# Performance work log

Hardware: AMD Instinct MI355X
Metric: run time of the kernel (lower is better)

## Reference

```python
import jax, jax.numpy as jnp
import numpy as np

N_NODES = 100000


def setup_inputs() -> dict:
    key = jax.random.key(0)
    k1, k2, k3 = jax.random.split(key, 3)
    x = jax.random.normal(k1, (N_NODES, 128), dtype=jnp.float32)
    edge_index = jax.random.randint(k2, (2, 1600000), 0, N_NODES, dtype=jnp.int32)
    # GCNConv linear weight: [out_features, in_features], bias: [out_features]
    W = jax.random.normal(k3, (128, 128), dtype=jnp.float32) * (1.0 / np.sqrt(128.0))
    b = jnp.zeros((128,), dtype=jnp.float32)
    return {"x": x, "edge_index": edge_index, "W": W, "b": b}


def reference(x, edge_index, W, b):
    n = x.shape[0]
    # --- add self loops (PyG GCNConv default) ---
    loop = jnp.arange(n, dtype=edge_index.dtype)
    row = jnp.concatenate([edge_index[0], loop])  # source nodes
    col = jnp.concatenate([edge_index[1], loop])  # target nodes
    # --- symmetric degree normalization D^{-1/2} A_hat D^{-1/2} ---
    ones = jnp.ones(row.shape[0], dtype=x.dtype)
    deg = jax.ops.segment_sum(ones, col, num_segments=n)
    deg_inv_sqrt = jnp.where(deg > 0, jax.lax.rsqrt(deg), 0.0)
    norm = deg_inv_sqrt[row] * deg_inv_sqrt[col]  # [E + N]
    # --- linear transform then gather-normalize-scatter aggregation ---
    xw = x @ W.T  # [N, out]
    msgs = xw[row] * norm[:, None]  # [E + N, out]
    out = jax.ops.segment_sum(msgs, col, num_segments=n)  # [N, out]
    return out + b
```

## Files before the change

### kernel.cpp

```cpp
#include <hip/hip_runtime.h>

#define NF 128
#define WLD2 136

#define BSHIFT 7
#define BNODES (1 << BSHIFT)
#define NBUCK 782
#define BCAP 2560
#define CHUNK 4096

typedef __attribute__((ext_vector_type(8))) short bf16x8;
typedef __attribute__((ext_vector_type(4))) float f32x4;

__device__ inline short f2bf_rne(float f) {
    unsigned u = __float_as_uint(f);
    u += 0x7FFFu + ((u >> 16) & 1u);
    return (short)(u >> 16);
}
__device__ inline float bf_lo(unsigned u) { return __uint_as_float(u << 16); }
__device__ inline float bf_hi(unsigned u) { return __uint_as_float(u & 0xFFFF0000u); }

__global__ void binit_kernel(int* __restrict__ bcursor) {
    int i = blockIdx.x * blockDim.x + threadIdx.x;
    if (i < NBUCK) bcursor[i] = i * BCAP;
}

__global__ __launch_bounds__(256) void bucketize_kernel(const int* __restrict__ row,
                                                        const int* __restrict__ col,
                                                        int* __restrict__ bcursor,
                                                        int* __restrict__ bpacked, int E) {
    __shared__ int2 pe[CHUNK];
    __shared__ int hist[NBUCK];
    __shared__ int base[NBUCK];
    const int t = threadIdx.x;
    const int e0 = blockIdx.x * CHUNK;
    const int cnt = min(CHUNK, E - e0);
    for (int i = t; i < NBUCK; i += 256) hist[i] = 0;
    __syncthreads();
    for (int i = t; i < cnt; i += 256) {
        int c = col[e0 + i];
        int r = row[e0 + i];
        pe[i] = make_int2(c, r);
        atomicAdd(&hist[c >> BSHIFT], 1);
    }
    __syncthreads();
    for (int i = t; i < NBUCK; i += 256) {
        int h = hist[i];
        base[i] = h ? atomicAdd(&bcursor[i], h) : 0;
        hist[i] = 0;
    }
    __syncthreads();
    for (int i = t; i < cnt; i += 256) {
        int2 p = pe[i];
        int bk = p.x >> BSHIFT;
        int pos = base[bk] + atomicAdd(&hist[bk], 1);
        bpacked[pos] = (p.y << BSHIFT) | (p.x & (BNODES - 1));
    }
}

__device__ inline int block_exclusive_scan_256(int val) {
    __shared__ int wsum[4];
    int lane = threadIdx.x & 63, wave = threadIdx.x >> 6;
    int x = val;
#pragma unroll
    for (int off = 1; off < 64; off <<= 1) {
        int y = __shfl_up(x, off, 64);
        if (lane >= off) x += y;
    }
    if (lane == 63) wsum[wave] = x;
    __syncthreads();
    if (threadIdx.x == 0) {
        int acc = 0;
        for (int w = 0; w < 4; ++w) { int t = wsum[w]; wsum[w] = acc; acc += t; }
    }
    __syncthreads();
    return x - val + wsum[wave];
}

__global__ __launch_bounds__(256) void bucket_build_kernel(const int* __restrict__ bpacked,
                                                           const int* __restrict__ bcursor,
                                                           int* __restrict__ cnt,
                                                           float* __restrict__ dis,
                                                           int* __restrict__ offs,
                                                           int* __restrict__ ed, int N) {
    __shared__ int pe[BCAP];
    __shared__ int h[BNODES];
    __shared__ int edl[BCAP];
    const int b = blockIdx.x;
    const int node0 = b << BSHIFT;
    const int nn = min(BNODES, N - node0);
    const int start = b * BCAP;
    const int ecnt = bcursor[b] - start;
    for (int i = threadIdx.x; i < nn; i += 256) h[i] = 0;
    __syncthreads();
    for (int i = threadIdx.x; i < ecnt; i += 256) {
        int p = bpacked[start + i];
        pe[i] = p;
        atomicAdd(&h[p & (BNODES - 1)], 1);
    }
    __syncthreads();
    const int t = threadIdx.x;
    int v0 = (2 * t < nn) ? h[2 * t] : 0;
    int v1 = (2 * t + 1 < nn) ? h[2 * t + 1] : 0;
    int exc = block_exclusive_scan_256(v0 + v1);
    if (2 * t < nn) {
        offs[node0 + 2 * t] = start + exc;
        cnt[node0 + 2 * t] = v0;
        dis[node0 + 2 * t] = rsqrtf((float)v0 + 1.0f);
        h[2 * t] = exc;
    }
    if (2 * t + 1 < nn) {
        offs[node0 + 2 * t + 1] = start + exc + v0;
        cnt[node0 + 2 * t + 1] = v1;
        dis[node0 + 2 * t + 1] = rsqrtf((float)v1 + 1.0f);
        h[2 * t + 1] = exc + v0;
    }
    __syncthreads();
    for (int i = threadIdx.x; i < ecnt; i += 256) {
        int p = pe[i];
        int pos = atomicAdd(&h[p & (BNODES - 1)], 1);
        edl[pos] = p >> BSHIFT;
    }
    __syncthreads();
    for (int i = threadIdx.x; i < ecnt; i += 256) ed[start + i] = edl[i];
}

__global__ __launch_bounds__(256) void gemm_xws_kernel(const float* __restrict__ x,
                                                       const float* __restrict__ W,
                                                       const float* __restrict__ dis,
                                                       unsigned short* __restrict__ xws,
                                                       int n) {
    __shared__ short Wl[NF * WLD2];

    for (int idx = threadIdx.x; idx < NF * 32; idx += 256) {
        int o = idx >> 5;
        int kq = (idx & 31) << 2;
        float4 v = *(const float4*)(W + o * NF + kq);
        short* d = &Wl[o * WLD2 + kq];
        d[0] = f2bf_rne(v.x); d[1] = f2bf_rne(v.y);
        d[2] = f2bf_rne(v.z); d[3] = f2bf_rne(v.w);
    }
    __syncthreads();

    const int lane = threadIdx.x & 63;
    const int wave = threadIdx.x >> 6;
    const int mbase = wave * 32;
    const int l15 = lane & 15;
    const int quad = lane >> 4;
    const int tile = blockIdx.x * 128;

    f32x4 acc[2][8];
#pragma unroll
    for (int mb = 0; mb < 2; ++mb)
#pragma unroll
        for (int nb = 0; nb < 8; ++nb) acc[mb][nb] = (f32x4)0.0f;

#pragma unroll
    for (int kc = 0; kc < 4; ++kc) {
        const int kof = kc * 32 + quad * 8;
        bf16x8 Bf[8];
#pragma unroll
        for (int nb = 0; nb < 8; ++nb) {
            int o = nb * 16 + l15;
            Bf[nb] = *(const bf16x8*)(&Wl[o * WLD2 + kof]);
        }
#pragma unroll
        for (int mb = 0; mb < 2; ++mb) {
            int r = tile + mbase + mb * 16 + l15;
            if (r >= n) r = n - 1;
            const float4* ap = (const float4*)(x + (size_t)r * NF + kof);
            float4 a0 = ap[0], a1 = ap[1];
            bf16x8 Af;
            Af[0] = f2bf_rne(a0.x); Af[1] = f2bf_rne(a0.y);
            Af[2] = f2bf_rne(a0.z); Af[3] = f2bf_rne(a0.w);
            Af[4] = f2bf_rne(a1.x); Af[5] = f2bf_rne(a1.y);
            Af[6] = f2bf_rne(a1.z); Af[7] = f2bf_rne(a1.w);
#pragma unroll
            for (int nb = 0; nb < 8; ++nb)
                acc[mb][nb] = __builtin_amdgcn_mfma_f32_16x16x32_bf16(Af, Bf[nb], acc[mb][nb], 0, 0, 0);
        }
    }

#pragma unroll
    for (int mb = 0; mb < 2; ++mb) {
        int rbase = tile + mbase + mb * 16 + quad * 4;
#pragma unroll
        for (int reg = 0; reg < 4; ++reg) {
            int r = rbase + reg;
            if (r < n) {
                float dsc = dis[r];
#pragma unroll
                for (int nb = 0; nb < 8; ++nb) {
                    int c = nb * 16 + l15;
                    xws[(size_t)r * NF + c] = (unsigned short)f2bf_rne(acc[mb][nb][reg] * dsc);
                }
            }
        }
    }
}

__global__ __launch_bounds__(256) void gather_kernel(const int* __restrict__ ed,
                                                     const int* __restrict__ offs,
                                                     const int* __restrict__ cnt,
                                                     const float* __restrict__ dis,
                                                     const unsigned short* __restrict__ xws,
                                                     const float* __restrict__ b,
                                                     float* __restrict__ out,
                                                     int nbase, int nend) {
    int node = nbase + (int)((blockIdx.x * blockDim.x + threadIdx.x) >> 6);
    const int lane = threadIdx.x & 63;
    if (node >= nend) return;
    node = __builtin_amdgcn_readfirstlane(node);
    const int lsub = lane & 31;
    const bool lo = lane < 32;
    const float dc = dis[node];
    const int start = offs[node];
    const int end = start + cnt[node];

    float ax = 0.f, ay = 0.f, az = 0.f, aw = 0.f;
    {
        uint2 u = *(const uint2*)(xws + (size_t)node * NF + lsub * 4);
        if (lo) { ax = bf_lo(u.x); ay = bf_hi(u.x); az = bf_lo(u.y); aw = bf_hi(u.y); }
    }
    int i = start;
    for (; i + 16 <= end; i += 16) {
        int r0 = ed[i], r1 = ed[i + 1], r2 = ed[i + 2], r3 = ed[i + 3];
        int r4 = ed[i + 4], r5 = ed[i + 5], r6 = ed[i + 6], r7 = ed[i + 7];
        int r8 = ed[i + 8], r9 = ed[i + 9], ra = ed[i + 10], rb = ed[i + 11];
        int rc = ed[i + 12], rd = ed[i + 13], re = ed[i + 14], rf = ed[i + 15];
        int sa = lo ? r0 : r1, sb = lo ? r2 : r3, sc = lo ? r4 : r5, sd = lo ? r6 : r7;
        int se = lo ? r8 : r9, sf = lo ? ra : rb, sg = lo ? rc : rd, sh = lo ? re : rf;
        uint2 ua = *(const uint2*)(xws + (size_t)sa * NF + lsub * 4);
        uint2 ub = *(const uint2*)(xws + (size_t)sb * NF + lsub * 4);
        uint2 uc = *(const uint2*)(xws + (size_t)sc * NF + lsub * 4);
        uint2 ud = *(const uint2*)(xws + (size_t)sd * NF + lsub * 4);
        uint2 ue = *(const uint2*)(xws + (size_t)se * NF + lsub * 4);
        uint2 uf = *(const uint2*)(xws + (size_t)sf * NF + lsub * 4);
        uint2 ug = *(const uint2*)(xws + (size_t)sg * NF + lsub * 4);
        uint2 uh = *(const uint2*)(xws + (size_t)sh * NF + lsub * 4);
        ax += bf_lo(ua.x) + bf_lo(ub.x) + bf_lo(uc.x) + bf_lo(ud.x);
        ay += bf_hi(ua.x) + bf_hi(ub.x) + bf_hi(uc.x) + bf_hi(ud.x);
        az += bf_lo(ua.y) + bf_lo(ub.y) + bf_lo(uc.y) + bf_lo(ud.y);
        aw += bf_hi(ua.y) + bf_hi(ub.y) + bf_hi(uc.y) + bf_hi(ud.y);
        ax += bf_lo(ue.x) + bf_lo(uf.x) + bf_lo(ug.x) + bf_lo(uh.x);
        ay += bf_hi(ue.x) + bf_hi(uf.x) + bf_hi(ug.x) + bf_hi(uh.x);
        az += bf_lo(ue.y) + bf_lo(uf.y) + bf_lo(ug.y) + bf_lo(uh.y);
        aw += bf_hi(ue.y) + bf_hi(uf.y) + bf_hi(ug.y) + bf_hi(uh.y);
    }
    for (; i < end; i += 8) {
        int i1 = min(i + 1, end - 1), i2 = min(i + 2, end - 1), i3 = min(i + 3, end - 1);
        int i4 = min(i + 4, end - 1), i5 = min(i + 5, end - 1), i6 = min(i + 6, end - 1),
            i7 = min(i + 7, end - 1);
        int r0 = ed[i], r1 = ed[i1], r2 = ed[i2], r3 = ed[i3];
        int r4 = ed[i4], r5 = ed[i5], r6 = ed[i6], r7 = ed[i7];
        int sa = lo ? r0 : r1, sb = lo ? r2 : r3, sc = lo ? r4 : r5, sd = lo ? r6 : r7;
        uint2 ua = *(const uint2*)(xws + (size_t)sa * NF + lsub * 4);
        uint2 ub = *(const uint2*)(xws + (size_t)sb * NF + lsub * 4);
        uint2 uc = *(const uint2*)(xws + (size_t)sc * NF + lsub * 4);
        uint2 ud = *(const uint2*)(xws + (size_t)sd * NF + lsub * 4);
        const int my0 = lo ? 0 : 1;
        if (i + my0 < end)     { ax += bf_lo(ua.x); ay += bf_hi(ua.x); az += bf_lo(ua.y); aw += bf_hi(ua.y); }
        if (i + 2 + my0 < end) { ax += bf_lo(ub.x); ay += bf_hi(ub.x); az += bf_lo(ub.y); aw += bf_hi(ub.y); }
        if (i + 4 + my0 < end) { ax += bf_lo(uc.x); ay += bf_hi(uc.x); az += bf_lo(uc.y); aw += bf_hi(uc.y); }
        if (i + 6 + my0 < end) { ax += bf_lo(ud.x); ay += bf_hi(ud.x); az += bf_lo(ud.y); aw += bf_hi(ud.y); }
    }
    ax += __shfl_xor(ax, 32, 64);
    ay += __shfl_xor(ay, 32, 64);
    az += __shfl_xor(az, 32, 64);
    aw += __shfl_xor(aw, 32, 64);
    if (lo) {
        float4 bb = ((const float4*)b)[lsub];
        float4 o;
        o.x = fmaf(ax, dc, bb.x);
        o.y = fmaf(ay, dc, bb.y);
        o.z = fmaf(az, dc, bb.z);
        o.w = fmaf(aw, dc, bb.w);
        ((float4*)(out + (size_t)node * NF))[lsub] = o;
    }
}

extern "C" void kernel_launch(void* const* d_in, const int* in_sizes, int n_in,
                              void* d_out, int out_size, void* d_ws, size_t ws_size,
                              hipStream_t stream) {
    const float* x = (const float*)d_in[0];
    const int* ei = (const int*)d_in[1];
    const float* W = (const float*)d_in[2];
    const float* b = (const float*)d_in[3];
    float* out = (float*)d_out;

    const int N = in_sizes[0] / NF;
    const int E = in_sizes[1] / 2;
    const int* row = ei;
    const int* col = ei + E;

    char* ws = (char*)d_ws;
    unsigned short* xws = (unsigned short*)ws;
    ws += (size_t)N * NF * sizeof(unsigned short);
    int* cnt = (int*)ws; ws += (size_t)N * sizeof(int);
    float* dis = (float*)ws; ws += (size_t)N * sizeof(float);
    int* offs = (int*)ws; ws += (size_t)N * sizeof(int);
    int* bpacked = (int*)ws; ws += (size_t)NBUCK * BCAP * sizeof(int);
    int* bcursor = (int*)ws; ws += 1024 * sizeof(int);
    int* ed = (int*)ws;

    const int CB = (E + CHUNK - 1) / CHUNK;

    binit_kernel<<<(NBUCK + 255) / 256, 256, 0, stream>>>(bcursor);
    bucketize_kernel<<<CB, 256, 0, stream>>>(row, col, bcursor, bpacked, E);

    bucket_build_kernel<<<NBUCK, 256, 0, stream>>>(bpacked, bcursor, cnt, dis, offs, ed, N);

    gemm_xws_kernel<<<(N + 127) / 128, 256, 0, stream>>>(x, W, dis, xws, N);

    {
        int half = (N / 2 + 3) & ~3;
        int blocks1 = (half + 3) / 4;
        int blocks2 = (N - half + 3) / 4;
        gather_kernel<<<blocks1, 256, 0, stream>>>(ed, offs, cnt, dis, xws, b, out, 0, half);
        gather_kernel<<<blocks2, 256, 0, stream>>>(ed, offs, cnt, dis, xws, b, out, half, N);
    }
}
```

Before: 220.0 us.

## Pre-swizzle bf16 weights once and shrink GEMM tiles to 64 rows

A prep kernel, folded into the bucket cursor init, converts W to bf16 once in MFMA fragment order. Each GEMM block then copies that swizzled layout into LDS with a plain vector copy, instead of converting fp32 W per block with padded strides. Each block now handles 64 rows with one 16-row MFMA tile per wave, and all x loads are issued up front. This is meant to cut per-block W conversion cost and register pressure and to improve occupancy and latency hiding. The cost is twice as many blocks, each reloading the 32KB W tile.

```diff
diff --git a/kernel.cpp b/kernel.cpp
--- a/kernel.cpp
+++ b/kernel.cpp
@@ -1,7 +1,6 @@
 #include <hip/hip_runtime.h>
 
 #define NF 128
-#define WLD2 136
 
 #define BSHIFT 7
 #define BNODES (1 << BSHIFT)
@@ -20,9 +19,25 @@
 __device__ inline float bf_lo(unsigned u) { return __uint_as_float(u << 16); }
 __device__ inline float bf_hi(unsigned u) { return __uint_as_float(u & 0xFFFF0000u); }
 
-__global__ void binit_kernel(int* __restrict__ bcursor) {
-    int i = blockIdx.x * blockDim.x + threadIdx.x;
-    if (i < NBUCK) bcursor[i] = i * BCAP;
+__global__ __launch_bounds__(256) void prep_kernel(const float* __restrict__ W,
+                                                   unsigned short* __restrict__ wswz,
+                                                   int* __restrict__ bcursor) {
+    int t = blockIdx.x * 256 + threadIdx.x;
+    if (t < NBUCK) bcursor[t] = t * BCAP;
+    if (t < 2048) {
+        int lane = t & 63, frag = t >> 6;
+        int nb = frag & 7, kc = frag >> 3;
+        int o = nb * 16 + (lane & 15);
+        int k0 = kc * 32 + (lane >> 4) * 8;
+        const float4* ap = (const float4*)(W + o * NF + k0);
+        float4 a0 = ap[0], a1 = ap[1];
+        bf16x8 v;
+        v[0] = f2bf_rne(a0.x); v[1] = f2bf_rne(a0.y);
+        v[2] = f2bf_rne(a0.z); v[3] = f2bf_rne(a0.w);
+        v[4] = f2bf_rne(a1.x); v[5] = f2bf_rne(a1.y);
+        v[6] = f2bf_rne(a1.z); v[7] = f2bf_rne(a1.w);
+        *(bf16x8*)(wswz + (size_t)t * 8) = v;
+    }
 }
 
 __global__ __launch_bounds__(256) void bucketize_kernel(const int* __restrict__ row,
@@ -126,75 +141,60 @@
 }
 
 __global__ __launch_bounds__(256) void gemm_xws_kernel(const float* __restrict__ x,
-                                                       const float* __restrict__ W,
+                                                       const unsigned short* __restrict__ wswz,
                                                        const float* __restrict__ dis,
                                                        unsigned short* __restrict__ xws,
                                                        int n) {
-    __shared__ short Wl[NF * WLD2];
-
-    for (int idx = threadIdx.x; idx < NF * 32; idx += 256) {
-        int o = idx >> 5;
-        int kq = (idx & 31) << 2;
-        float4 v = *(const float4*)(W + o * NF + kq);
-        short* d = &Wl[o * WLD2 + kq];
-        d[0] = f2bf_rne(v.x); d[1] = f2bf_rne(v.y);
-        d[2] = f2bf_rne(v.z); d[3] = f2bf_rne(v.w);
-    }
+    __shared__ short Wl[NF * NF];
+
+    for (int i = threadIdx.x; i < NF * NF / 8; i += 256)
+        *(bf16x8*)(&Wl[i * 8]) = *(const bf16x8*)(wswz + (size_t)i * 8);
     __syncthreads();
 
     const int lane = threadIdx.x & 63;
     const int wave = threadIdx.x >> 6;
-    const int mbase = wave * 32;
     const int l15 = lane & 15;
     const int quad = lane >> 4;
-    const int tile = blockIdx.x * 128;
-
-    f32x4 acc[2][8];
-#pragma unroll
-    for (int mb = 0; mb < 2; ++mb)
-#pragma unroll
-        for (int nb = 0; nb < 8; ++nb) acc[mb][nb] = (f32x4)0.0f;
-
+    const int tile = blockIdx.x * 64;
+
+    int r = tile + wave * 16 + l15;
+    if (r >= n) r = n - 1;
+
+    float4 xa[4][2];
 #pragma unroll
     for (int kc = 0; kc < 4; ++kc) {
-        const int kof = kc * 32 + quad * 8;
-        bf16x8 Bf[8];
+        const float4* ap = (const float4*)(x + (size_t)r * NF + kc * 32 + quad * 8);
+        xa[kc][0] = ap[0];
+        xa[kc][1] = ap[1];
+    }
+
+    f32x4 acc[8];
+#pragma unroll
+    for (int nb = 0; nb < 8; ++nb) acc[nb] = (f32x4)0.0f;
+
+#pragma unroll
+    for (int kc = 0; kc < 4; ++kc) {
+        bf16x8 Af;
+        Af[0] = f2bf_rne(xa[kc][0].x); Af[1] = f2bf_rne(xa[kc][0].y);
+        Af[2] = f2bf_rne(xa[kc][0].z); Af[3] = f2bf_rne(xa[kc][0].w);
+        Af[4] = f2bf_rne(xa[kc][1].x); Af[5] = f2bf_rne(xa[kc][1].y);
+        Af[6] = f2bf_rne(xa[kc][1].z); Af[7] = f2bf_rne(xa[kc][1].w);
 #pragma unroll
         for (int nb = 0; nb < 8; ++nb) {
-            int o = nb * 16 + l15;
-            Bf[nb] = *(const bf16x8*)(&Wl[o * WLD2 + kof]);
+            bf16x8 Bf = *(const bf16x8*)(&Wl[((kc * 8 + nb) * 64 + lane) * 8]);
+            acc[nb] = __builtin_amdgcn_mfma_f32_16x16x32_bf16(Af, Bf, acc[nb], 0, 0, 0);
         }
-#pragma unroll
-        for (int mb = 0; mb < 2; ++mb) {
-            int r = tile + mbase + mb * 16 + l15;
-            if (r >= n) r = n - 1;
-            const float4* ap = (const float4*)(x + (size_t)r * NF + kof);
-            float4 a0 = ap[0], a1 = ap[1];
-            bf16x8 Af;
-            Af[0] = f2bf_rne(a0.x); Af[1] = f2bf_rne(a0.y);
-            Af[2] = f2bf_rne(a0.z); Af[3] = f2bf_rne(a0.w);
-            Af[4] = f2bf_rne(a1.x); Af[5] = f2bf_rne(a1.y);
-            Af[6] = f2bf_rne(a1.z); Af[7] = f2bf_rne(a1.w);
+    }
+
+    int rbase = tile + wave * 16 + quad * 4;
+#pragma unroll
+    for (int reg = 0; reg < 4; ++reg) {
+        int rr = rbase + reg;
+        if (rr < n) {
+            float dsc = dis[rr];
 #pragma unroll
             for (int nb = 0; nb < 8; ++nb)
-                acc[mb][nb] = __builtin_amdgcn_mfma_f32_16x16x32_bf16(Af, Bf[nb], acc[mb][nb], 0, 0, 0);
-        }
-    }
-
-#pragma unroll
-    for (int mb = 0; mb < 2; ++mb) {
-        int rbase = tile + mbase + mb * 16 + quad * 4;
-#pragma unroll
-        for (int reg = 0; reg < 4; ++reg) {
-            int r = rbase + reg;
-            if (r < n) {
-                float dsc = dis[r];
-#pragma unroll
-                for (int nb = 0; nb < 8; ++nb) {
-                    int c = nb * 16 + l15;
-                    xws[(size_t)r * NF + c] = (unsigned short)f2bf_rne(acc[mb][nb][reg] * dsc);
-                }
-            }
+                xws[(size_t)rr * NF + nb * 16 + l15] = (unsigned short)f2bf_rne(acc[nb][reg] * dsc);
         }
     }
 }
@@ -299,18 +299,19 @@
     int* cnt = (int*)ws; ws += (size_t)N * sizeof(int);
     float* dis = (float*)ws; ws += (size_t)N * sizeof(float);
     int* offs = (int*)ws; ws += (size_t)N * sizeof(int);
+    unsigned short* wswz = (unsigned short*)ws; ws += (size_t)NF * NF * sizeof(unsigned short);
     int* bpacked = (int*)ws; ws += (size_t)NBUCK * BCAP * sizeof(int);
     int* bcursor = (int*)ws; ws += 1024 * sizeof(int);
     int* ed = (int*)ws;
 
     const int CB = (E + CHUNK - 1) / CHUNK;
 
-    binit_kernel<<<(NBUCK + 255) / 256, 256, 0, stream>>>(bcursor);
+    prep_kernel<<<8, 256, 0, stream>>>(W, wswz, bcursor);
     bucketize_kernel<<<CB, 256, 0, stream>>>(row, col, bcursor, bpacked, E);
 
     bucket_build_kernel<<<NBUCK, 256, 0, stream>>>(bpacked, bcursor, cnt, dis, offs, ed, N);
 
-    gemm_xws_kernel<<<(N + 127) / 128, 256, 0, stream>>>(x, W, dis, xws, N);
+    gemm_xws_kernel<<<(N + 63) / 64, 256, 0, stream>>>(x, wswz, dis, xws, N);
 
     {
         int half = (N / 2 + 3) & ~3;
```

After: 214.1 us. -2.7%, faster.
